# Kernel optimization log

Hardware: AMD Instinct MI355X
Metric: run time of the kernel (lower is better)

## Reference

```python
import jax, jax.numpy as jnp
import numpy as np

B, N, M = 2, 8192, 8192
PEN_RATIO = 0.95
REG_W = 0.001
LOSS_W = 1.0
EPS_COS = 1e-8


def quat_to_rot(q):
    # q: [..., 4] in (x, y, z, w) order (legacy kornia convention), assumed normalized
    x, y, z, w = q[..., 0], q[..., 1], q[..., 2], q[..., 3]
    r0 = jnp.stack([1 - 2 * (y * y + z * z), 2 * (x * y - z * w), 2 * (x * z + y * w)], -1)
    r1 = jnp.stack([2 * (x * y + z * w), 1 - 2 * (x * x + z * z), 2 * (y * z - x * w)], -1)
    r2 = jnp.stack([2 * (x * z - y * w), 2 * (y * z + x * w), 1 - 2 * (x * x + y * y)], -1)
    return jnp.stack([r0, r1, r2], -2)


def span_cov(cp):
    # cp: [N,7] -> SPD cov [N,3,3]; eigenvalues are cumulative sums (e0, e0+e1, e0+e1+e2)
    e0 = cp[:, 0]
    e1 = e0 + cp[:, 1]
    e2 = e1 + cp[:, 2]
    eig = jnp.stack([e0, e1, e2], -1)  # [N,3]
    q = cp[:, 3:] / (jnp.linalg.norm(cp[:, 3:], axis=-1, keepdims=True) + 1e-9)
    E = quat_to_rot(q)  # [N,3,3]
    return jnp.einsum('nij,nj,nkj->nik', E, eig, E)


def setup_inputs() -> dict:
    key = jax.random.key(0)
    ks = jax.random.split(key, 8)
    return {
        'xyz_pred': jax.random.normal(ks[0], (B, N, 3), jnp.float32) * 10.0,
        'xyz_target': jax.random.normal(ks[1], (B, M, 3), jnp.float32) * 10.0,
        'cov_pred': jax.random.uniform(ks[2], (B, N, 7), jnp.float32),
        'cov_target': jax.random.uniform(ks[3], (B, M, 7), jnp.float32),
        'R_pred': jax.random.normal(ks[4], (B, 3, 3), jnp.float32),
        't_pred': jax.random.normal(ks[5], (B, 3), jnp.float32),
        'normal_pred': jax.random.normal(ks[6], (B, N, 3), jnp.float32),
        'normal_target': jax.random.normal(ks[7], (B, M, 3), jnp.float32),
    }


def reference(xyz_pred, xyz_target, cov_pred, cov_target, R_pred, t_pred, normal_pred, normal_target):
    def per_batch(xp, xt, cp, ct, R, nrm):
        covp = span_cov(cp)  # [N,3,3]
        covt = span_cov(ct)  # [M,3,3]
        # one-direction chamfer: squared NN distance + index (||p||^2+||t||^2-2 p.t)
        d2 = (xp * xp).sum(-1)[:, None] + (xt * xt).sum(-1)[None, :] - 2.0 * (xp @ xt.T)  # [N,M]
        diff = d2.min(axis=1)          # [N]
        idx = jnp.argmin(d2, axis=1)   # [N]
        xa = xt[idx]                   # associated target points
        cpa = covt[idx]                # associated target covariances
        dv = xp - xa
        # ROI mask via kth value: k = 1 + int(N*ratio) (1-indexed) -> sorted[int(N*ratio)]
        m = jnp.maximum(jnp.sort(diff)[int(N * PEN_RATIO)], 1.0)
        cm = (diff < m).astype(xp.dtype)
        nvalid = cm.sum()
        Rd = jax.lax.stop_gradient(R)
        sigma = covp + jnp.einsum('ij,njk,lk->nil', Rd, cpa, Rd)
        sigma_inv = jnp.linalg.inv(sigma)
        sq = jnp.einsum('ni,nij,nj->n', dv, sigma_inv, dv)  # Mahalanobis sq dist
        logdet = jnp.log(jnp.linalg.det(sigma))
        loss_b = (sq * cm).sum() / nvalid + REG_W * (0.5 * logdet * cm).sum() / nvalid
        # weighted SVD registration head (single ICP iter), all detached as in torch
        diff_na = xa - xp
        cossim = (nrm * diff_na).sum(-1) / jnp.maximum(
            jnp.linalg.norm(nrm, axis=-1) * jnp.linalg.norm(diff_na, axis=-1), EPS_COS)
        w = jax.lax.stop_gradient(jnp.abs(cossim) ** 2 * cm)
        src = jax.lax.stop_gradient(xp)
        tgt = jax.lax.stop_gradient(xa)
        wn = w / w.sum()
        sc = (wn[:, None] * src).sum(0)
        tc = (wn[:, None] * tgt).sum(0)
        H = jnp.einsum('n,ni,nj->ij', w, src - sc, tgt - tc)
        U, S, Vt = jnp.linalg.svd(H)
        V = Vt.T
        d = jnp.linalg.det(V @ U.T)
        Rres = V @ jnp.diag(jnp.stack([jnp.ones_like(d), jnp.ones_like(d), d])) @ U.T
        tres = tc - Rres @ sc
        return loss_b, Rres, tres

    losses, Rs, ts = jax.vmap(per_batch)(xyz_pred, xyz_target, cov_pred, cov_target, R_pred, normal_pred)
    return LOSS_W * losses.sum(), Rs, ts
```

## Files before the change

### kernel.cpp

```cpp
#include <hip/hip_runtime.h>
#include <math.h>

#define B_ 2
#define N_ 8192
#define M_ 8192
#define KSEL 7782
#define CH 128
#define CHS (M_ / CH)
#define PTS 1024
#define PPT 4

__device__ __forceinline__ unsigned ord_of(float f) {
  unsigned u = __float_as_uint(f);
  return (u & 0x80000000u) ? ~u : (u | 0x80000000u);
}
__device__ __forceinline__ float float_of_ord(unsigned o) {
  unsigned u = (o & 0x80000000u) ? (o ^ 0x80000000u) : ~o;
  return __uint_as_float(u);
}

__global__ __launch_bounds__(256) void init_kernel(
    unsigned long long* __restrict__ keys, const float* __restrict__ xt,
    float* __restrict__ tnorm) {
  const int gid = blockIdx.x * 256 + threadIdx.x;
  keys[gid] = 0xFFFFFFFFFFFFFFFFull;
  float tx = xt[gid * 3 + 0], ty = xt[gid * 3 + 1], tz = xt[gid * 3 + 2];
  tnorm[gid] = tx * tx + ty * ty + tz * tz;
}

__global__ __launch_bounds__(256, 8) void nn_kernel(
    const float* __restrict__ xp, const float* __restrict__ xt,
    const float* __restrict__ tnorm, unsigned long long* __restrict__ keys) {
  const int b = blockIdx.z;
  const int pblk = blockIdx.x;
  const int ch = blockIdx.y;

  __shared__ float4 tg[CHS];
  const float* __restrict__ xtb = xt + ((size_t)b * M_ + (size_t)ch * CHS) * 3;
  const float* __restrict__ twb = tnorm + (size_t)b * M_ + (size_t)ch * CHS;
  if (threadIdx.x < CHS) {
    const int j = threadIdx.x;
    tg[j] = make_float4(xtb[3 * j + 0], xtb[3 * j + 1], xtb[3 * j + 2],
                        twb[j]);
  }
  __syncthreads();

  const int i0 = pblk * PTS + threadIdx.x;
  float xm[PPT], ym[PPT], zm[PPT], nrm2[PPT], best[PPT];
  int bi[PPT];
#pragma unroll
  for (int k = 0; k < PPT; ++k) {
    const float* p = xp + ((size_t)b * N_ + i0 + k * 256) * 3;
    float x = p[0], y = p[1], z = p[2];
    nrm2[k] = x * x + y * y + z * z;
    xm[k] = -2.0f * x;
    ym[k] = -2.0f * y;
    zm[k] = -2.0f * z;
    best[k] = 3.4e38f;
    bi[k] = 0;
  }

#pragma unroll 2
  for (int j = 0; j < CHS; ++j) {
    float4 t = tg[j];
#pragma unroll
    for (int k = 0; k < PPT; ++k) {
      float d = fmaf(t.x, xm[k], fmaf(t.y, ym[k], fmaf(t.z, zm[k], t.w)));
      if (d < best[k]) { best[k] = d; bi[k] = j; }
    }
  }

  const int base = ch * CHS;
#pragma unroll
  for (int k = 0; k < PPT; ++k) {
    unsigned long long key =
        ((unsigned long long)ord_of(best[k] + nrm2[k]) << 32) |
        (unsigned)(base + bi[k]);
    atomicMin(&keys[(size_t)b * N_ + i0 + k * 256], key);
  }
}

__global__ __launch_bounds__(1024) void sel_kernel(
    const unsigned long long* __restrict__ keys, float* __restrict__ mout,
    double* __restrict__ acc) {
  __shared__ unsigned hist[256];
  __shared__ unsigned sel_digit, sel_rank;
  const int b = blockIdx.x;

  if (threadIdx.x < 32) acc[b * 32 + threadIdx.x] = 0.0;

  unsigned v[8];
#pragma unroll
  for (int t = 0; t < 8; ++t)
    v[t] = (unsigned)(keys[(size_t)b * N_ + threadIdx.x + t * 1024] >> 32);

  unsigned prefix = 0;
  unsigned rank = KSEL;

#pragma unroll
  for (int pass = 0; pass < 4; ++pass) {
    const int shift = 24 - pass * 8;
    const unsigned pmask = (pass == 0) ? 0u : (0xFFFFFFFFu << (shift + 8));

    if (threadIdx.x < 256) hist[threadIdx.x] = 0;
    __syncthreads();

#pragma unroll
    for (int t = 0; t < 8; ++t) {
      if ((v[t] & pmask) == prefix)
        atomicAdd(&hist[(v[t] >> shift) & 0xFFu], 1u);
    }
    __syncthreads();

    if (threadIdx.x < 64) {
      const int lane = threadIdx.x;
      unsigned h0 = hist[lane * 4 + 0], h1 = hist[lane * 4 + 1];
      unsigned h2 = hist[lane * 4 + 2], h3 = hist[lane * 4 + 3];
      unsigned c0 = h0, c1 = c0 + h1, c2 = c1 + h2, c3 = c2 + h3;
      unsigned s = c3;
#pragma unroll
      for (int off = 1; off < 64; off <<= 1) {
        unsigned t = __shfl_up(s, off);
        if (lane >= off) s += t;
      }
      unsigned excl = s - c3;
      unsigned r = rank;
      if (r >= excl && r < excl + c0) { sel_digit = lane * 4 + 0; sel_rank = r - excl; }
      if (r >= excl + c0 && r < excl + c1) { sel_digit = lane * 4 + 1; sel_rank = r - (excl + c0); }
      if (r >= excl + c1 && r < excl + c2) { sel_digit = lane * 4 + 2; sel_rank = r - (excl + c1); }
      if (r >= excl + c2 && r < excl + c3) { sel_digit = lane * 4 + 3; sel_rank = r - (excl + c2); }
    }
    __syncthreads();
    prefix |= (sel_digit << shift);
    rank = sel_rank;
    __syncthreads();
  }

  if (threadIdx.x == 0) {
    float f = float_of_ord(prefix);
    mout[b] = fmaxf(f, 1.0f);
  }
}

__device__ __forceinline__ void cov_from_params(const float* __restrict__ c,
                                                float C[3][3]) {
  float e0 = c[0];
  float e1 = e0 + c[1];
  float e2 = e1 + c[2];
  float qx = c[3], qy = c[4], qz = c[5], qw = c[6];
  float qn = sqrtf(qx * qx + qy * qy + qz * qz + qw * qw) + 1e-9f;
  float x = qx / qn, y = qy / qn, z = qz / qn, w = qw / qn;
  float E[3][3];
  E[0][0] = 1.0f - 2.0f * (y * y + z * z);
  E[0][1] = 2.0f * (x * y - z * w);
  E[0][2] = 2.0f * (x * z + y * w);
  E[1][0] = 2.0f * (x * y + z * w);
  E[1][1] = 1.0f - 2.0f * (x * x + z * z);
  E[1][2] = 2.0f * (y * z - x * w);
  E[2][0] = 2.0f * (x * z - y * w);
  E[2][1] = 2.0f * (y * z + x * w);
  E[2][2] = 1.0f - 2.0f * (x * x + y * y);
#pragma unroll
  for (int i = 0; i < 3; ++i)
#pragma unroll
    for (int k = 0; k < 3; ++k)
      C[i][k] = e0 * E[i][0] * E[k][0] + e1 * E[i][1] * E[k][1] +
                e2 * E[i][2] * E[k][2];
}

__global__ __launch_bounds__(256) void main_kernel(
    const float* __restrict__ xp, const float* __restrict__ xt,
    const float* __restrict__ cpp, const float* __restrict__ ctp,
    const float* __restrict__ Rp, const float* __restrict__ nrm,
    const unsigned long long* __restrict__ keys, const float* __restrict__ mout,
    double* __restrict__ acc) {
  const int b = blockIdx.y;
  const int i = blockIdx.x * 256 + threadIdx.x;

  float R[3][3];
#pragma unroll
  for (int r = 0; r < 3; ++r)
#pragma unroll
    for (int c = 0; c < 3; ++c) R[r][c] = Rp[b * 9 + r * 3 + c];
  const float m = mout[b];

  unsigned long long key = keys[(size_t)b * N_ + i];
  float d2 = float_of_ord((unsigned)(key >> 32));
  int id = (int)(key & 0xFFFFFFFFull);

  const float* p = xp + ((size_t)b * N_ + i) * 3;
  float px = p[0], py = p[1], pz = p[2];
  const float* a_ = xt + ((size_t)b * M_ + id) * 3;
  float ax = a_[0], ay = a_[1], az = a_[2];

  float cmv = (d2 < m) ? 1.0f : 0.0f;

  float Cp[3][3], Ct[3][3];
  cov_from_params(cpp + ((size_t)b * N_ + i) * 7, Cp);
  cov_from_params(ctp + ((size_t)b * M_ + id) * 7, Ct);

  float T[3][3], G[3][3];
#pragma unroll
  for (int r = 0; r < 3; ++r)
#pragma unroll
    for (int c = 0; c < 3; ++c)
      T[r][c] = R[r][0] * Ct[0][c] + R[r][1] * Ct[1][c] + R[r][2] * Ct[2][c];
#pragma unroll
  for (int r = 0; r < 3; ++r)
#pragma unroll
    for (int c = 0; c < 3; ++c)
      G[r][c] = Cp[r][c] +
                (T[r][0] * R[c][0] + T[r][1] * R[c][1] + T[r][2] * R[c][2]);

  float c00 = G[1][1] * G[2][2] - G[1][2] * G[2][1];
  float c01 = G[1][2] * G[2][0] - G[1][0] * G[2][2];
  float c02 = G[1][0] * G[2][1] - G[1][1] * G[2][0];
  float det = G[0][0] * c00 + G[0][1] * c01 + G[0][2] * c02;
  float rdet = 1.0f / det;
  float i00 = (G[1][1] * G[2][2] - G[1][2] * G[2][1]) * rdet;
  float i01 = (G[0][2] * G[2][1] - G[0][1] * G[2][2]) * rdet;
  float i02 = (G[0][1] * G[1][2] - G[0][2] * G[1][1]) * rdet;
  float i10 = (G[1][2] * G[2][0] - G[1][0] * G[2][2]) * rdet;
  float i11 = (G[0][0] * G[2][2] - G[0][2] * G[2][0]) * rdet;
  float i12 = (G[0][2] * G[1][0] - G[0][0] * G[1][2]) * rdet;
  float i20 = (G[1][0] * G[2][1] - G[1][1] * G[2][0]) * rdet;
  float i21 = (G[0][1] * G[2][0] - G[0][0] * G[2][1]) * rdet;
  float i22 = (G[0][0] * G[1][1] - G[0][1] * G[1][0]) * rdet;

  float dvx = px - ax, dvy = py - ay, dvz = pz - az;
  float t0 = i00 * dvx + i01 * dvy + i02 * dvz;
  float t1 = i10 * dvx + i11 * dvy + i12 * dvz;
  float t2 = i20 * dvx + i21 * dvy + i22 * dvz;
  float sq = dvx * t0 + dvy * t1 + dvz * t2;
  float logdet = logf(det);

  const float* nv = nrm + ((size_t)b * N_ + i) * 3;
  float nx = nv[0], ny = nv[1], nz = nv[2];
  float gx = ax - px, gy = ay - py, gz = az - pz;
  float dt = nx * gx + ny * gy + nz * gz;
  float den = fmaxf(sqrtf(nx * nx + ny * ny + nz * nz) *
                        sqrtf(gx * gx + gy * gy + gz * gz),
                    1e-8f);
  float cs = dt / den;
  float w = cs * cs * cmv;

  double vals[19];
  vals[0] = (double)cmv;
  vals[1] = (double)(sq) * (double)cmv;
  vals[2] = (double)(logdet) * (double)cmv;
  vals[3] = (double)w;
  vals[4] = (double)w * px;
  vals[5] = (double)w * py;
  vals[6] = (double)w * pz;
  vals[7] = (double)w * ax;
  vals[8] = (double)w * ay;
  vals[9] = (double)w * az;
  float pr[3] = {px, py, pz}, ar[3] = {ax, ay, az};
#pragma unroll
  for (int r = 0; r < 3; ++r)
#pragma unroll
    for (int c = 0; c < 3; ++c)
      vals[10 + r * 3 + c] = (double)w * (double)pr[r] * (double)ar[c];

#pragma unroll
  for (int off = 32; off > 0; off >>= 1) {
#pragma unroll
    for (int k = 0; k < 19; ++k) vals[k] += __shfl_down(vals[k], off);
  }
  __shared__ double red[4][19];
  const int lane = threadIdx.x & 63, wv = threadIdx.x >> 6;
  if (lane == 0) {
#pragma unroll
    for (int k = 0; k < 19; ++k) red[wv][k] = vals[k];
  }
  __syncthreads();
  if (threadIdx.x < 19) {
    double s = red[0][threadIdx.x] + red[1][threadIdx.x] +
               red[2][threadIdx.x] + red[3][threadIdx.x];
    atomicAdd(&acc[b * 32 + threadIdx.x], s);
  }
}

__device__ float det3f(const float M[3][3]) {
  return M[0][0] * (M[1][1] * M[2][2] - M[1][2] * M[2][1]) -
         M[0][1] * (M[1][0] * M[2][2] - M[1][2] * M[2][0]) +
         M[0][2] * (M[1][0] * M[2][1] - M[1][1] * M[2][0]);
}

__device__ void eigvec3f(const float A[3][3], float lam, float v[3]) {
  float r[3][3];
#pragma unroll
  for (int i = 0; i < 3; ++i) {
#pragma unroll
    for (int j = 0; j < 3; ++j) r[i][j] = A[i][j];
    r[i][i] -= lam;
  }
  float c01[3] = {r[0][1] * r[1][2] - r[0][2] * r[1][1],
                  r[0][2] * r[1][0] - r[0][0] * r[1][2],
                  r[0][0] * r[1][1] - r[0][1] * r[1][0]};
  float c02[3] = {r[0][1] * r[2][2] - r[0][2] * r[2][1],
                  r[0][2] * r[2][0] - r[0][0] * r[2][2],
                  r[0][0] * r[2][1] - r[0][1] * r[2][0]};
  float c12[3] = {r[1][1] * r[2][2] - r[1][2] * r[2][1],
                  r[1][2] * r[2][0] - r[1][0] * r[2][2],
                  r[1][0] * r[2][1] - r[1][1] * r[2][0]};
  float n01 = c01[0] * c01[0] + c01[1] * c01[1] + c01[2] * c01[2];
  float n02 = c02[0] * c02[0] + c02[1] * c02[1] + c02[2] * c02[2];
  float n12 = c12[0] * c12[0] + c12[1] * c12[1] + c12[2] * c12[2];
  float* best = c01;
  float bn = n01;
  if (n02 > bn) { best = c02; bn = n02; }
  if (n12 > bn) { best = c12; bn = n12; }
  float inv = (bn > 0.0f) ? 1.0f / sqrtf(bn) : 0.0f;
  v[0] = best[0] * inv;
  v[1] = best[1] * inv;
  v[2] = best[2] * inv;
  if (inv == 0.0f) v[0] = 1.0f;
}

__device__ void kabschf(const float H[3][3], float R[3][3]) {
  float A[3][3];
  for (int i = 0; i < 3; ++i)
    for (int j = 0; j < 3; ++j)
      A[i][j] = H[0][i] * H[0][j] + H[1][i] * H[1][j] + H[2][i] * H[2][j];

  float lam[3];
  float Vs[3][3];
  float mtr = (A[0][0] + A[1][1] + A[2][2]) / 3.0f;
  float K00 = A[0][0] - mtr, K11 = A[1][1] - mtr, K22 = A[2][2] - mtr;
  float a01 = A[0][1], a02 = A[0][2], a12 = A[1][2];
  float p2 = K00 * K00 + K11 * K11 + K22 * K22 +
             2.0f * (a01 * a01 + a02 * a02 + a12 * a12);
  float p = sqrtf(p2 / 6.0f);
  if (p < 1e-12f) {
    lam[0] = lam[1] = lam[2] = mtr;
    for (int i = 0; i < 3; ++i)
      for (int j = 0; j < 3; ++j) Vs[i][j] = (i == j) ? 1.0f : 0.0f;
  } else {
    float detK = K00 * (K11 * K22 - a12 * a12) -
                 a01 * (a01 * K22 - a12 * a02) +
                 a02 * (a01 * a12 - K11 * a02);
    float rr = detK / (2.0f * p * p * p);
    rr = fminf(1.0f, fmaxf(-1.0f, rr));
    float phi = acosf(rr) / 3.0f;
    lam[0] = mtr + 2.0f * p * cosf(phi);
    lam[2] = mtr + 2.0f * p * cosf(phi + 2.0943951023931953f);
    lam[1] = 3.0f * mtr - lam[0] - lam[2];

    float v0[3], v1[3];
    eigvec3f(A, lam[0], v0);
    eigvec3f(A, lam[1], v1);
    float dp = v1[0] * v0[0] + v1[1] * v0[1] + v1[2] * v0[2];
    v1[0] -= dp * v0[0];
    v1[1] -= dp * v0[1];
    v1[2] -= dp * v0[2];
    float n1 = v1[0] * v1[0] + v1[1] * v1[1] + v1[2] * v1[2];
    if (n1 > 1e-20f) {
      float inv = 1.0f / sqrtf(n1);
      v1[0] *= inv; v1[1] *= inv; v1[2] *= inv;
    } else {
      float ax = fabsf(v0[0]), ay = fabsf(v0[1]), az = fabsf(v0[2]);
      float t[3] = {0.0f, 0.0f, 0.0f};
      if (ax <= ay && ax <= az) t[0] = 1.0f;
      else if (ay <= az) t[1] = 1.0f;
      else t[2] = 1.0f;
      v1[0] = v0[1] * t[2] - v0[2] * t[1];
      v1[1] = v0[2] * t[0] - v0[0] * t[2];
      v1[2] = v0[0] * t[1] - v0[1] * t[0];
      float inv = 1.0f / sqrtf(v1[0] * v1[0] + v1[1] * v1[1] + v1[2] * v1[2]);
      v1[0] *= inv; v1[1] *= inv; v1[2] *= inv;
    }
    float v2[3] = {v0[1] * v1[2] - v0[2] * v1[1],
                   v0[2] * v1[0] - v0[0] * v1[2],
                   v0[0] * v1[1] - v0[1] * v1[0]};
    for (int i = 0; i < 3; ++i) {
      Vs[i][0] = v0[i];
      Vs[i][1] = v1[i];
      Vs[i][2] = v2[i];
    }
  }

  float sg[3];
  for (int c = 0; c < 3; ++c) sg[c] = sqrtf(fmaxf(lam[c], 0.0f));

  float U[3][3];
  for (int c = 0; c < 3; ++c) {
    float ux = H[0][0] * Vs[0][c] + H[0][1] * Vs[1][c] + H[0][2] * Vs[2][c];
    float uy = H[1][0] * Vs[0][c] + H[1][1] * Vs[1][c] + H[1][2] * Vs[2][c];
    float uz = H[2][0] * Vs[0][c] + H[2][1] * Vs[1][c] + H[2][2] * Vs[2][c];
    float inv = (sg[c] > 1e-6f * sg[0] + 1e-30f) ? 1.0f / sg[c] : 0.0f;
    U[0][c] = ux * inv;
    U[1][c] = uy * inv;
    U[2][c] = uz * inv;
  }
  if (sg[2] <= 1e-6f * sg[0] + 1e-30f) {
    U[0][2] = U[1][0] * U[2][1] - U[2][0] * U[1][1];
    U[1][2] = U[2][0] * U[0][1] - U[0][0] * U[2][1];
    U[2][2] = U[0][0] * U[1][1] - U[1][0] * U[0][1];
  }
  float d = det3f(U) * det3f(Vs);
  for (int i = 0; i < 3; ++i)
    for (int j = 0; j < 3; ++j)
      R[i][j] = Vs[i][0] * U[j][0] + Vs[i][1] * U[j][1] + d * Vs[i][2] * U[j][2];
}

__global__ __launch_bounds__(64) void finalize_kernel(
    const double* __restrict__ acc, float* __restrict__ out) {
  __shared__ double lossb[B_];
  const int b = threadIdx.x;
  if (b < B_) {
    const double* a = acc + b * 32;
    double cnt = a[0], ssq = a[1], sld = a[2], W = a[3];
    double loss = ssq / cnt + 0.001 * 0.5 * sld / cnt;
    lossb[b] = loss;
    double Ss[3] = {a[4], a[5], a[6]}, St[3] = {a[7], a[8], a[9]};
    double sc[3], tc[3];
    for (int c = 0; c < 3; ++c) { sc[c] = Ss[c] / W; tc[c] = St[c] / W; }
    double H[3][3];
    double hmax = 1e-30;
    for (int i = 0; i < 3; ++i)
      for (int j = 0; j < 3; ++j) {
        H[i][j] = a[10 + i * 3 + j] - Ss[i] * St[j] / W;
        double ab = fabs(H[i][j]);
        if (ab > hmax) hmax = ab;
      }
    float Hf[3][3];
    double rinv = 1.0 / hmax;
    for (int i = 0; i < 3; ++i)
      for (int j = 0; j < 3; ++j) Hf[i][j] = (float)(H[i][j] * rinv);
    float Rf[3][3];
    kabschf(Hf, Rf);
    for (int i = 0; i < 3; ++i)
      for (int j = 0; j < 3; ++j)
        out[1 + b * 9 + i * 3 + j] = Rf[i][j];
    for (int i = 0; i < 3; ++i) {
      double t = tc[i] - ((double)Rf[i][0] * sc[0] + (double)Rf[i][1] * sc[1] +
                          (double)Rf[i][2] * sc[2]);
      out[1 + B_ * 9 + b * 3 + i] = (float)t;
    }
  }
  __syncthreads();
  if (threadIdx.x == 0) out[0] = (float)(lossb[0] + lossb[1]);
}

extern "C" void kernel_launch(void* const* d_in, const int* in_sizes, int n_in,
                              void* d_out, int out_size, void* d_ws,
                              size_t ws_size, hipStream_t stream) {
  const float* xyz_pred = (const float*)d_in[0];
  const float* xyz_target = (const float*)d_in[1];
  const float* cov_pred = (const float*)d_in[2];
  const float* cov_target = (const float*)d_in[3];
  const float* R_pred = (const float*)d_in[4];
  const float* normal_pred = (const float*)d_in[6];
  float* out = (float*)d_out;

  char* ws = (char*)d_ws;
  double* acc = (double*)ws;
  unsigned long long* keys = (unsigned long long*)(ws + 512);
  float* mout = (float*)(ws + 512 + (size_t)B_ * N_ * 8);
  float* tnorm = (float*)(ws + 1024 + (size_t)B_ * N_ * 8);

  hipLaunchKernelGGL(init_kernel, dim3(B_ * M_ / 256), dim3(256), 0, stream,
                     keys, xyz_target, tnorm);
  hipLaunchKernelGGL(nn_kernel, dim3(N_ / PTS, CH, B_), dim3(256), 0, stream,
                     xyz_pred, xyz_target, tnorm, keys);
  hipLaunchKernelGGL(sel_kernel, dim3(B_), dim3(1024), 0, stream, keys, mout,
                     acc);
  hipLaunchKernelGGL(main_kernel, dim3(N_ / 256, B_), dim3(256), 0, stream,
                     xyz_pred, xyz_target, cov_pred, cov_target, R_pred,
                     normal_pred, keys, mout, acc);
  hipLaunchKernelGGL(finalize_kernel, dim3(1), dim3(64), 0, stream, acc, out);
}
```

Measured before the change: 45.80 us.

## Fuse selection, main and finalize kernels into one tail kernel with flags

Merges the radix-select kernel, the per-point loss/accumulation kernel and the finalize kernel into a single launch. One extra block per batch computes the threshold and publishes it through a release-store flag, while the other blocks spin on it. A last-block-done counter then runs the Kabsch finalize. This removes two kernel launches and their gaps. In exchange the selection block now has only 256 threads doing 32 loads each, and the design relies on the selector block being co-resident with the spinning blocks to avoid deadlock.

```diff
diff --git a/kernel.cpp b/kernel.cpp
--- a/kernel.cpp
+++ b/kernel.cpp
@@ -21,11 +21,15 @@
 
 __global__ __launch_bounds__(256) void init_kernel(
     unsigned long long* __restrict__ keys, const float* __restrict__ xt,
-    float* __restrict__ tnorm) {
+    float* __restrict__ tnorm, double* __restrict__ acc,
+    unsigned* __restrict__ flag, unsigned* __restrict__ done) {
   const int gid = blockIdx.x * 256 + threadIdx.x;
   keys[gid] = 0xFFFFFFFFFFFFFFFFull;
   float tx = xt[gid * 3 + 0], ty = xt[gid * 3 + 1], tz = xt[gid * 3 + 2];
   tnorm[gid] = tx * tx + ty * ty + tz * tz;
+  if (gid < B_ * 32) acc[gid] = 0.0;
+  if (gid < B_) flag[gid] = 0u;
+  if (gid == B_) *done = 0u;
 }
 
 __global__ __launch_bounds__(256, 8) void nn_kernel(
@@ -77,68 +81,6 @@
         ((unsigned long long)ord_of(best[k] + nrm2[k]) << 32) |
         (unsigned)(base + bi[k]);
     atomicMin(&keys[(size_t)b * N_ + i0 + k * 256], key);
-  }
-}
-
-__global__ __launch_bounds__(1024) void sel_kernel(
-    const unsigned long long* __restrict__ keys, float* __restrict__ mout,
-    double* __restrict__ acc) {
-  __shared__ unsigned hist[256];
-  __shared__ unsigned sel_digit, sel_rank;
-  const int b = blockIdx.x;
-
-  if (threadIdx.x < 32) acc[b * 32 + threadIdx.x] = 0.0;
-
-  unsigned v[8];
-#pragma unroll
-  for (int t = 0; t < 8; ++t)
-    v[t] = (unsigned)(keys[(size_t)b * N_ + threadIdx.x + t * 1024] >> 32);
-
-  unsigned prefix = 0;
-  unsigned rank = KSEL;
-
-#pragma unroll
-  for (int pass = 0; pass < 4; ++pass) {
-    const int shift = 24 - pass * 8;
-    const unsigned pmask = (pass == 0) ? 0u : (0xFFFFFFFFu << (shift + 8));
-
-    if (threadIdx.x < 256) hist[threadIdx.x] = 0;
-    __syncthreads();
-
-#pragma unroll
-    for (int t = 0; t < 8; ++t) {
-      if ((v[t] & pmask) == prefix)
-        atomicAdd(&hist[(v[t] >> shift) & 0xFFu], 1u);
-    }
-    __syncthreads();
-
-    if (threadIdx.x < 64) {
-      const int lane = threadIdx.x;
-      unsigned h0 = hist[lane * 4 + 0], h1 = hist[lane * 4 + 1];
-      unsigned h2 = hist[lane * 4 + 2], h3 = hist[lane * 4 + 3];
-      unsigned c0 = h0, c1 = c0 + h1, c2 = c1 + h2, c3 = c2 + h3;
-      unsigned s = c3;
-#pragma unroll
-      for (int off = 1; off < 64; off <<= 1) {
-        unsigned t = __shfl_up(s, off);
-        if (lane >= off) s += t;
-      }
-      unsigned excl = s - c3;
-      unsigned r = rank;
-      if (r >= excl && r < excl + c0) { sel_digit = lane * 4 + 0; sel_rank = r - excl; }
-      if (r >= excl + c0 && r < excl + c1) { sel_digit = lane * 4 + 1; sel_rank = r - (excl + c0); }
-      if (r >= excl + c1 && r < excl + c2) { sel_digit = lane * 4 + 2; sel_rank = r - (excl + c1); }
-      if (r >= excl + c2 && r < excl + c3) { sel_digit = lane * 4 + 3; sel_rank = r - (excl + c2); }
-    }
-    __syncthreads();
-    prefix |= (sel_digit << shift);
-    rank = sel_rank;
-    __syncthreads();
-  }
-
-  if (threadIdx.x == 0) {
-    float f = float_of_ord(prefix);
-    mout[b] = fmaxf(f, 1.0f);
   }
 }
 
@@ -166,119 +108,6 @@
     for (int k = 0; k < 3; ++k)
       C[i][k] = e0 * E[i][0] * E[k][0] + e1 * E[i][1] * E[k][1] +
                 e2 * E[i][2] * E[k][2];
-}
-
-__global__ __launch_bounds__(256) void main_kernel(
-    const float* __restrict__ xp, const float* __restrict__ xt,
-    const float* __restrict__ cpp, const float* __restrict__ ctp,
-    const float* __restrict__ Rp, const float* __restrict__ nrm,
-    const unsigned long long* __restrict__ keys, const float* __restrict__ mout,
-    double* __restrict__ acc) {
-  const int b = blockIdx.y;
-  const int i = blockIdx.x * 256 + threadIdx.x;
-
-  float R[3][3];
-#pragma unroll
-  for (int r = 0; r < 3; ++r)
-#pragma unroll
-    for (int c = 0; c < 3; ++c) R[r][c] = Rp[b * 9 + r * 3 + c];
-  const float m = mout[b];
-
-  unsigned long long key = keys[(size_t)b * N_ + i];
-  float d2 = float_of_ord((unsigned)(key >> 32));
-  int id = (int)(key & 0xFFFFFFFFull);
-
-  const float* p = xp + ((size_t)b * N_ + i) * 3;
-  float px = p[0], py = p[1], pz = p[2];
-  const float* a_ = xt + ((size_t)b * M_ + id) * 3;
-  float ax = a_[0], ay = a_[1], az = a_[2];
-
-  float cmv = (d2 < m) ? 1.0f : 0.0f;
-
-  float Cp[3][3], Ct[3][3];
-  cov_from_params(cpp + ((size_t)b * N_ + i) * 7, Cp);
-  cov_from_params(ctp + ((size_t)b * M_ + id) * 7, Ct);
-
-  float T[3][3], G[3][3];
-#pragma unroll
-  for (int r = 0; r < 3; ++r)
-#pragma unroll
-    for (int c = 0; c < 3; ++c)
-      T[r][c] = R[r][0] * Ct[0][c] + R[r][1] * Ct[1][c] + R[r][2] * Ct[2][c];
-#pragma unroll
-  for (int r = 0; r < 3; ++r)
-#pragma unroll
-    for (int c = 0; c < 3; ++c)
-      G[r][c] = Cp[r][c] +
-                (T[r][0] * R[c][0] + T[r][1] * R[c][1] + T[r][2] * R[c][2]);
-
-  float c00 = G[1][1] * G[2][2] - G[1][2] * G[2][1];
-  float c01 = G[1][2] * G[2][0] - G[1][0] * G[2][2];
-  float c02 = G[1][0] * G[2][1] - G[1][1] * G[2][0];
-  float det = G[0][0] * c00 + G[0][1] * c01 + G[0][2] * c02;
-  float rdet = 1.0f / det;
-  float i00 = (G[1][1] * G[2][2] - G[1][2] * G[2][1]) * rdet;
-  float i01 = (G[0][2] * G[2][1] - G[0][1] * G[2][2]) * rdet;
-  float i02 = (G[0][1] * G[1][2] - G[0][2] * G[1][1]) * rdet;
-  float i10 = (G[1][2] * G[2][0] - G[1][0] * G[2][2]) * rdet;
-  float i11 = (G[0][0] * G[2][2] - G[0][2] * G[2][0]) * rdet;
-  float i12 = (G[0][2] * G[1][0] - G[0][0] * G[1][2]) * rdet;
-  float i20 = (G[1][0] * G[2][1] - G[1][1] * G[2][0]) * rdet;
-  float i21 = (G[0][1] * G[2][0] - G[0][0] * G[2][1]) * rdet;
-  float i22 = (G[0][0] * G[1][1] - G[0][1] * G[1][0]) * rdet;
-
-  float dvx = px - ax, dvy = py - ay, dvz = pz - az;
-  float t0 = i00 * dvx + i01 * dvy + i02 * dvz;
-  float t1 = i10 * dvx + i11 * dvy + i12 * dvz;
-  float t2 = i20 * dvx + i21 * dvy + i22 * dvz;
-  float sq = dvx * t0 + dvy * t1 + dvz * t2;
-  float logdet = logf(det);
-
-  const float* nv = nrm + ((size_t)b * N_ + i) * 3;
-  float nx = nv[0], ny = nv[1], nz = nv[2];
-  float gx = ax - px, gy = ay - py, gz = az - pz;
-  float dt = nx * gx + ny * gy + nz * gz;
-  float den = fmaxf(sqrtf(nx * nx + ny * ny + nz * nz) *
-                        sqrtf(gx * gx + gy * gy + gz * gz),
-                    1e-8f);
-  float cs = dt / den;
-  float w = cs * cs * cmv;
-
-  double vals[19];
-  vals[0] = (double)cmv;
-  vals[1] = (double)(sq) * (double)cmv;
-  vals[2] = (double)(logdet) * (double)cmv;
-  vals[3] = (double)w;
-  vals[4] = (double)w * px;
-  vals[5] = (double)w * py;
-  vals[6] = (double)w * pz;
-  vals[7] = (double)w * ax;
-  vals[8] = (double)w * ay;
-  vals[9] = (double)w * az;
-  float pr[3] = {px, py, pz}, ar[3] = {ax, ay, az};
-#pragma unroll
-  for (int r = 0; r < 3; ++r)
-#pragma unroll
-    for (int c = 0; c < 3; ++c)
-      vals[10 + r * 3 + c] = (double)w * (double)pr[r] * (double)ar[c];
-
-#pragma unroll
-  for (int off = 32; off > 0; off >>= 1) {
-#pragma unroll
-    for (int k = 0; k < 19; ++k) vals[k] += __shfl_down(vals[k], off);
-  }
-  __shared__ double red[4][19];
-  const int lane = threadIdx.x & 63, wv = threadIdx.x >> 6;
-  if (lane == 0) {
-#pragma unroll
-    for (int k = 0; k < 19; ++k) red[wv][k] = vals[k];
-  }
-  __syncthreads();
-  if (threadIdx.x < 19) {
-    double s = red[0][threadIdx.x] + red[1][threadIdx.x] +
-               red[2][threadIdx.x] + red[3][threadIdx.x];
-    atomicAdd(&acc[b * 32 + threadIdx.x], s);
-  }
 }
 
 __device__ float det3f(const float M[3][3]) {
@@ -404,39 +233,221 @@
       R[i][j] = Vs[i][0] * U[j][0] + Vs[i][1] * U[j][1] + d * Vs[i][2] * U[j][2];
 }
 
-__global__ __launch_bounds__(64) void finalize_kernel(
-    const double* __restrict__ acc, float* __restrict__ out) {
+__global__ __launch_bounds__(256) void tail_kernel(
+    const float* __restrict__ xp, const float* __restrict__ xt,
+    const float* __restrict__ cpp, const float* __restrict__ ctp,
+    const float* __restrict__ Rp, const float* __restrict__ nrm,
+    const unsigned long long* __restrict__ keys, double* __restrict__ acc,
+    unsigned* __restrict__ flag, unsigned* __restrict__ done,
+    float* __restrict__ out) {
+  const int b = blockIdx.y;
+
+  __shared__ unsigned hist[256];
+  __shared__ unsigned sel_digit, sel_rank;
+
+  if (blockIdx.x == 32) {
+    unsigned prefix = 0, rank = KSEL;
+    for (int pass = 0; pass < 4; ++pass) {
+      const int shift = 24 - pass * 8;
+      const unsigned pmask = (pass == 0) ? 0u : (0xFFFFFFFFu << (shift + 8));
+      hist[threadIdx.x] = 0;
+      __syncthreads();
+      for (int t = 0; t < 32; ++t) {
+        unsigned v =
+            (unsigned)(keys[(size_t)b * N_ + threadIdx.x + t * 256] >> 32);
+        if ((v & pmask) == prefix)
+          atomicAdd(&hist[(v >> shift) & 0xFFu], 1u);
+      }
+      __syncthreads();
+      if (threadIdx.x < 64) {
+        const int lane = threadIdx.x;
+        unsigned h0 = hist[lane * 4 + 0], h1 = hist[lane * 4 + 1];
+        unsigned h2 = hist[lane * 4 + 2], h3 = hist[lane * 4 + 3];
+        unsigned c0 = h0, c1 = c0 + h1, c2 = c1 + h2, c3 = c2 + h3;
+        unsigned s = c3;
+#pragma unroll
+        for (int off = 1; off < 64; off <<= 1) {
+          unsigned t = __shfl_up(s, off);
+          if (lane >= off) s += t;
+        }
+        unsigned excl = s - c3;
+        unsigned r = rank;
+        if (r >= excl && r < excl + c0) { sel_digit = lane * 4 + 0; sel_rank = r - excl; }
+        if (r >= excl + c0 && r < excl + c1) { sel_digit = lane * 4 + 1; sel_rank = r - (excl + c0); }
+        if (r >= excl + c1 && r < excl + c2) { sel_digit = lane * 4 + 2; sel_rank = r - (excl + c1); }
+        if (r >= excl + c2 && r < excl + c3) { sel_digit = lane * 4 + 3; sel_rank = r - (excl + c2); }
+      }
+      __syncthreads();
+      prefix |= (sel_digit << shift);
+      rank = sel_rank;
+      __syncthreads();
+    }
+    if (threadIdx.x == 0) {
+      float m = fmaxf(float_of_ord(prefix), 1.0f);
+      __hip_atomic_store(&flag[b], __float_as_uint(m), __ATOMIC_RELEASE,
+                         __HIP_MEMORY_SCOPE_AGENT);
+    }
+    return;
+  }
+
+  __shared__ float m_sh;
+  if (threadIdx.x == 0) {
+    unsigned u;
+    while ((u = __hip_atomic_load(&flag[b], __ATOMIC_ACQUIRE,
+                                  __HIP_MEMORY_SCOPE_AGENT)) == 0u)
+      __builtin_amdgcn_s_sleep(16);
+    m_sh = __uint_as_float(u);
+  }
+  __syncthreads();
+  const float m = m_sh;
+
+  const int i = blockIdx.x * 256 + threadIdx.x;
+
+  float R[3][3];
+#pragma unroll
+  for (int r = 0; r < 3; ++r)
+#pragma unroll
+    for (int c = 0; c < 3; ++c) R[r][c] = Rp[b * 9 + r * 3 + c];
+
+  unsigned long long key = keys[(size_t)b * N_ + i];
+  float d2 = float_of_ord((unsigned)(key >> 32));
+  int id = (int)(key & 0xFFFFFFFFull);
+
+  const float* p = xp + ((size_t)b * N_ + i) * 3;
+  float px = p[0], py = p[1], pz = p[2];
+  const float* a_ = xt + ((size_t)b * M_ + id) * 3;
+  float ax = a_[0], ay = a_[1], az = a_[2];
+
+  float cmv = (d2 < m) ? 1.0f : 0.0f;
+
+  float Cp[3][3], Ct[3][3];
+  cov_from_params(cpp + ((size_t)b * N_ + i) * 7, Cp);
+  cov_from_params(ctp + ((size_t)b * M_ + id) * 7, Ct);
+
+  float T[3][3], G[3][3];
+#pragma unroll
+  for (int r = 0; r < 3; ++r)
+#pragma unroll
+    for (int c = 0; c < 3; ++c)
+      T[r][c] = R[r][0] * Ct[0][c] + R[r][1] * Ct[1][c] + R[r][2] * Ct[2][c];
+#pragma unroll
+  for (int r = 0; r < 3; ++r)
+#pragma unroll
+    for (int c = 0; c < 3; ++c)
+      G[r][c] = Cp[r][c] +
+                (T[r][0] * R[c][0] + T[r][1] * R[c][1] + T[r][2] * R[c][2]);
+
+  float c00 = G[1][1] * G[2][2] - G[1][2] * G[2][1];
+  float c01 = G[1][2] * G[2][0] - G[1][0] * G[2][2];
+  float c02 = G[1][0] * G[2][1] - G[1][1] * G[2][0];
+  float det = G[0][0] * c00 + G[0][1] * c01 + G[0][2] * c02;
+  float rdet = 1.0f / det;
+  float i00 = (G[1][1] * G[2][2] - G[1][2] * G[2][1]) * rdet;
+  float i01 = (G[0][2] * G[2][1] - G[0][1] * G[2][2]) * rdet;
+  float i02 = (G[0][1] * G[1][2] - G[0][2] * G[1][1]) * rdet;
+  float i10 = (G[1][2] * G[2][0] - G[1][0] * G[2][2]) * rdet;
+  float i11 = (G[0][0] * G[2][2] - G[0][2] * G[2][0]) * rdet;
+  float i12 = (G[0][2] * G[1][0] - G[0][0] * G[1][2]) * rdet;
+  float i20 = (G[1][0] * G[2][1] - G[1][1] * G[2][0]) * rdet;
+  float i21 = (G[0][1] * G[2][0] - G[0][0] * G[2][1]) * rdet;
+  float i22 = (G[0][0] * G[1][1] - G[0][1] * G[1][0]) * rdet;
+
+  float dvx = px - ax, dvy = py - ay, dvz = pz - az;
+  float t0 = i00 * dvx + i01 * dvy + i02 * dvz;
+  float t1 = i10 * dvx + i11 * dvy + i12 * dvz;
+  float t2 = i20 * dvx + i21 * dvy + i22 * dvz;
+  float sq = dvx * t0 + dvy * t1 + dvz * t2;
+  float logdet = logf(det);
+
+  const float* nv = nrm + ((size_t)b * N_ + i) * 3;
+  float nx = nv[0], ny = nv[1], nz = nv[2];
+  float gx = ax - px, gy = ay - py, gz = az - pz;
+  float dt = nx * gx + ny * gy + nz * gz;
+  float den = fmaxf(sqrtf(nx * nx + ny * ny + nz * nz) *
+                        sqrtf(gx * gx + gy * gy + gz * gz),
+                    1e-8f);
+  float cs = dt / den;
+  float w = cs * cs * cmv;
+
+  double vals[19];
+  vals[0] = (double)cmv;
+  vals[1] = (double)(sq) * (double)cmv;
+  vals[2] = (double)(logdet) * (double)cmv;
+  vals[3] = (double)w;
+  vals[4] = (double)w * px;
+  vals[5] = (double)w * py;
+  vals[6] = (double)w * pz;
+  vals[7] = (double)w * ax;
+  vals[8] = (double)w * ay;
+  vals[9] = (double)w * az;
+  float pr[3] = {px, py, pz}, ar[3] = {ax, ay, az};
+#pragma unroll
+  for (int r = 0; r < 3; ++r)
+#pragma unroll
+    for (int c = 0; c < 3; ++c)
+      vals[10 + r * 3 + c] = (double)w * (double)pr[r] * (double)ar[c];
+
+#pragma unroll
+  for (int off = 32; off > 0; off >>= 1) {
+#pragma unroll
+    for (int k = 0; k < 19; ++k) vals[k] += __shfl_down(vals[k], off);
+  }
+  __shared__ double red[4][19];
+  const int lane = threadIdx.x & 63, wv = threadIdx.x >> 6;
+  if (lane == 0) {
+#pragma unroll
+    for (int k = 0; k < 19; ++k) red[wv][k] = vals[k];
+  }
+  __syncthreads();
+  if (threadIdx.x < 19) {
+    double s = red[0][threadIdx.x] + red[1][threadIdx.x] +
+               red[2][threadIdx.x] + red[3][threadIdx.x];
+    atomicAdd(&acc[b * 32 + threadIdx.x], s);
+  }
+
+  __shared__ bool amLast;
+  __threadfence();
+  if (threadIdx.x == 0) {
+    unsigned old = atomicAdd(done, 1u);
+    amLast = (old == 32u * B_ - 1u);
+  }
+  __syncthreads();
+  if (!amLast) return;
+  __threadfence();
+
   __shared__ double lossb[B_];
-  const int b = threadIdx.x;
-  if (b < B_) {
-    const double* a = acc + b * 32;
+  const int fb = threadIdx.x;
+  if (fb < B_) {
+    double a[19];
+#pragma unroll
+    for (int k = 0; k < 19; ++k)
+      a[k] = atomicAdd(&acc[fb * 32 + k], 0.0);
     double cnt = a[0], ssq = a[1], sld = a[2], W = a[3];
-    double loss = ssq / cnt + 0.001 * 0.5 * sld / cnt;
-    lossb[b] = loss;
+    lossb[fb] = ssq / cnt + 0.001 * 0.5 * sld / cnt;
     double Ss[3] = {a[4], a[5], a[6]}, St[3] = {a[7], a[8], a[9]};
     double sc[3], tc[3];
     for (int c = 0; c < 3; ++c) { sc[c] = Ss[c] / W; tc[c] = St[c] / W; }
     double H[3][3];
     double hmax = 1e-30;
-    for (int i = 0; i < 3; ++i)
-      for (int j = 0; j < 3; ++j) {
-        H[i][j] = a[10 + i * 3 + j] - Ss[i] * St[j] / W;
-        double ab = fabs(H[i][j]);
+    for (int r = 0; r < 3; ++r)
+      for (int c = 0; c < 3; ++c) {
+        H[r][c] = a[10 + r * 3 + c] - Ss[r] * St[c] / W;
+        double ab = fabs(H[r][c]);
         if (ab > hmax) hmax = ab;
       }
     float Hf[3][3];
     double rinv = 1.0 / hmax;
-    for (int i = 0; i < 3; ++i)
-      for (int j = 0; j < 3; ++j) Hf[i][j] = (float)(H[i][j] * rinv);
+    for (int r = 0; r < 3; ++r)
+      for (int c = 0; c < 3; ++c) Hf[r][c] = (float)(H[r][c] * rinv);
     float Rf[3][3];
     kabschf(Hf, Rf);
-    for (int i = 0; i < 3; ++i)
-      for (int j = 0; j < 3; ++j)
-        out[1 + b * 9 + i * 3 + j] = Rf[i][j];
-    for (int i = 0; i < 3; ++i) {
-      double t = tc[i] - ((double)Rf[i][0] * sc[0] + (double)Rf[i][1] * sc[1] +
-                          (double)Rf[i][2] * sc[2]);
-      out[1 + B_ * 9 + b * 3 + i] = (float)t;
+    for (int r = 0; r < 3; ++r)
+      for (int c = 0; c < 3; ++c)
+        out[1 + fb * 9 + r * 3 + c] = Rf[r][c];
+    for (int r = 0; r < 3; ++r) {
+      double t = tc[r] - ((double)Rf[r][0] * sc[0] + (double)Rf[r][1] * sc[1] +
+                          (double)Rf[r][2] * sc[2]);
+      out[1 + B_ * 9 + fb * 3 + r] = (float)t;
     }
   }
   __syncthreads();
@@ -456,18 +467,16 @@
 
   char* ws = (char*)d_ws;
   double* acc = (double*)ws;
-  unsigned long long* keys = (unsigned long long*)(ws + 512);
-  float* mout = (float*)(ws + 512 + (size_t)B_ * N_ * 8);
+  unsigned* flag = (unsigned*)(ws + 512);
+  unsigned* done = (unsigned*)(ws + 512 + 64);
+  unsigned long long* keys = (unsigned long long*)(ws + 1024);
   float* tnorm = (float*)(ws + 1024 + (size_t)B_ * N_ * 8);
 
   hipLaunchKernelGGL(init_kernel, dim3(B_ * M_ / 256), dim3(256), 0, stream,
-                     keys, xyz_target, tnorm);
+                     keys, xyz_target, tnorm, acc, flag, done);
   hipLaunchKernelGGL(nn_kernel, dim3(N_ / PTS, CH, B_), dim3(256), 0, stream,
                      xyz_pred, xyz_target, tnorm, keys);
-  hipLaunchKernelGGL(sel_kernel, dim3(B_), dim3(1024), 0, stream, keys, mout,
-                     acc);
-  hipLaunchKernelGGL(main_kernel, dim3(N_ / 256, B_), dim3(256), 0, stream,
+  hipLaunchKernelGGL(tail_kernel, dim3(33, B_), dim3(256), 0, stream,
                      xyz_pred, xyz_target, cov_pred, cov_target, R_pred,
-                     normal_pred, keys, mout, acc);
-  hipLaunchKernelGGL(finalize_kernel, dim3(1), dim3(64), 0, stream, acc, out);
-}
+                     normal_pred, keys, acc, flag, done, out);
+}
```

New measurement: 67.11 us. 46.5% more time.
